# Performance work log

Hardware: AMD Instinct MI355X
Metric: run time of the kernel (lower is better)

The kernel has to match this reference:

```python
import jax, jax.numpy as jnp
import numpy as np

B, R, N, M, K = 4, 4, 4096, 64, 3
F_NUM = 512
KN = K * N


def _block(x, Ws, bs):
    """SO-Net PointResNet: 1x1 convs + ReLU; last layer sees concat(input, hidden)."""
    h = x
    for W, b in zip(Ws[:-1], bs[:-1]):
        h = jax.nn.relu(jnp.einsum('oc,bcn->bon', W, h) + b[None, :, None])
    h = jnp.concatenate([x, h], axis=1)
    return jax.nn.relu(jnp.einsum('oc,bcn->bon', Ws[-1], h) + bs[-1][None, :, None])


def _forward(x, intensity, node, node_knn_I, fpW, fpB, gpW, gpB):
    # --- som.query_topk: k nearest SOM nodes per point ---
    xd = jax.lax.stop_gradient(x)
    dist = jnp.sum((xd[:, :, :, None] - node[:, :, None, :]) ** 2, axis=1)      # B,N,M
    _, topk = jax.lax.top_k(-dist, K)                                           # B,N,K
    min_idx = topk.transpose(0, 2, 1).reshape(B, KN)                            # B,KN (k copies stacked)
    mask = jax.nn.one_hot(min_idx, M, dtype=jnp.float32)                        # B,KN,M
    mask_row_max = jnp.max(mask, axis=1) > 0                                    # B,M  node has >=1 point
    mask_row_sum = jnp.sum(mask, axis=1)                                        # B,M  points per node

    x_stack = jnp.tile(x, (1, 1, K))                                            # B,2,KN
    cluster_mean = jnp.einsum('bcn,bnm->bcm', jax.lax.stop_gradient(x_stack), mask) \
                   / (mask_row_sum[:, None, :] + 1e-5)                          # B,2,M (detached)

    # --- rotation group (2x2 rotations at angles 2*pi*r/R) ---
    theta = 2.0 * jnp.pi * jnp.arange(R, dtype=jnp.float32) / R
    c, s = jnp.cos(theta), jnp.sin(theta)
    rot = jnp.stack([jnp.stack([c, -s], -1), jnp.stack([s, c], -1)], -2)        # R,2,2

    x_rot = jnp.einsum('rij,bjn->brin', rot, x_stack)                           # B,R,2,KN
    node_rot = jnp.einsum('rij,bjm->brim', rot, cluster_mean)                   # B,R,2,M
    centers = jnp.take_along_axis(node_rot, min_idx[:, None, None, :], axis=3)  # B,R,2,KN
    x_dec = jax.lax.stop_gradient(x_rot - centers).reshape(B * R, 2, KN)

    # --- first PointResNet over all B*R rotation copies ---
    feat = _block(x_dec, fpW, fpB)                                              # BR,128,KN

    # --- index_max scatter-max per SOM cluster (value of argmax == segment max) ---
    seg = jnp.tile(min_idx[:, None, :], (1, R, 1)).reshape(B * R, KN)
    segmax = jax.vmap(lambda f, sgi: jax.ops.segment_max(f.T, sgi, num_segments=M).T)(feat, seg)
    rowmax = jnp.tile(mask_row_max[:, None, :], (1, R, 1)).reshape(B * R, M)
    pooled = jnp.where(rowmax[:, None, :], segmax, feat[:, :, 0:1])             # BR,128,M (empty -> gather idx 0)

    # --- final PointResNet over SOM nodes, then max over nodes and rotations ---
    g_in = jnp.concatenate([node_rot.reshape(B * R, 2, M), pooled], axis=1)     # BR,130,M
    out = _block(g_in, gpW, gpB)                                                # BR,F,M
    return out.reshape(B, R, F_NUM, M).max(axis=3).max(axis=1)                  # B,F


def setup_inputs() -> dict:
    key = jax.random.key(0)
    ks = jax.random.split(key, 24)
    d = {}
    d['x'] = jax.random.normal(ks[0], (B, 2, N), jnp.float32)
    d['intensity'] = jax.random.uniform(ks[1], (B, 1, N), jnp.float32)
    d['node'] = jax.random.normal(ks[2], (B, 2, M), jnp.float32)
    d['node_knn_I'] = jax.random.randint(ks[3], (B, M, 1), 0, M)
    dims_fp = [(64, 2), (64, 64), (128, 64), (128, 130)]      # PointResNet(2,[64,64,128,128])
    dims_gp = [(256, 130), (256, 256), (512, 256), (F_NUM, 642)]  # PointResNet(130,[256,256,512,F])
    i = 4
    for name, dims in (('fp', dims_fp), ('gp', dims_gp)):
        for j, (o, ci) in enumerate(dims):
            d[f'{name}_W{j}'] = jax.random.normal(ks[i], (o, ci), jnp.float32) / np.sqrt(ci).astype(np.float32)
            d[f'{name}_b{j}'] = jnp.zeros((o,), jnp.float32)
            i += 1
    return d


def reference(x, intensity, node, node_knn_I,
              fp_W0, fp_b0, fp_W1, fp_b1, fp_W2, fp_b2, fp_W3, fp_b3,
              gp_W0, gp_b0, gp_W1, gp_b1, gp_W2, gp_b2, gp_W3, gp_b3):
    return _forward(x, intensity, node, node_knn_I,
                    [fp_W0, fp_W1, fp_W2, fp_W3], [fp_b0, fp_b1, fp_b2, fp_b3],
                    [gp_W0, gp_W1, gp_W2, gp_W3], [gp_b0, gp_b1, gp_b2, gp_b3])
```

## Files before the change

### kernel.cpp

```cpp
#include <hip/hip_runtime.h>
#include <stdint.h>

#define BB 4
#define RR 4
#define NN 4096
#define MM 64
#define KK 3
#define KNN 12288
#define BRR 16
#define FF 512

#define W_FPW1 0
#define W_FPW2 4096
#define W_FPW3 12288
#define W_GPW0 28928
#define W_GPW1 62208
#define W_GPW2 127744
#define W_GPW3 258816
#define W_FPB1 587520
#define W_FPB2 587584
#define W_FPB3 587712
#define W_GPB0 587840
#define W_GPB1 588096
#define W_GPB2 588352
#define W_GPB3 588864
#define W_FPB0 589376
#define W_FPW0 589440
#define W_TOT  589568

typedef short bf16x8 __attribute__((ext_vector_type(8)));
typedef float f32x4 __attribute__((ext_vector_type(4)));

__device__ __forceinline__ float bf2f(unsigned int u) {
  union { unsigned int i; float f; } v; v.i = u << 16; return v.f;
}
__device__ __forceinline__ unsigned short f2bf(float f) {
  union { float f; unsigned int i; } v; v.f = f;
  unsigned int x = v.i;
  return (unsigned short)((x + 0x7fffu + ((x >> 16) & 1u)) >> 16);
}
__device__ __forceinline__ unsigned int f2bf2(float a, float b) {
#if __has_builtin(__builtin_amdgcn_cvt_pk_bf16_f32)
  typedef __bf16 bf2_t __attribute__((ext_vector_type(2)));
  union { bf2_t v; unsigned int u; } c;
  c.v = __builtin_amdgcn_cvt_pk_bf16_f32(a, b);
  return c.u;
#else
  return (unsigned int)f2bf(a) | ((unsigned int)f2bf(b) << 16);
#endif
}
__device__ __forceinline__ float ldf(const void* p, long i, int isbf) {
  if (isbf) return bf2f(((const unsigned short*)p)[i]);
  return ((const float*)p)[i];
}
__device__ __forceinline__ int detect_bf(const unsigned short* xs) {
  int lane = threadIdx.x & 63;
  unsigned short u = xs[lane * 2];
  int e = (u >> 7) & 0xFF;
  int bad = (e >= 0x90 || (e > 0 && e <= 0x50)) ? 1 : 0;
  unsigned long long m = __ballot(bad);
  return __popcll(m) < 16;
}

struct SrcPtrs { const void* p[16]; };
__global__ __launch_bounds__(256) void k_pre(
    SrcPtrs sp, const void* __restrict__ x, const void* __restrict__ node,
    int* __restrict__ idx, float* __restrict__ csum, int* __restrict__ blkcnt,
    unsigned short* __restrict__ Wb, unsigned long long* __restrict__ pooled64) {
  int isbf = detect_bf((const unsigned short*)x);
  int tid = threadIdx.x;
  if (blockIdx.x >= 64) {
    int zb = blockIdx.x - 64;
    if (zb < 256) pooled64[zb * 256 + tid] = 0ull;
    int t2 = zb * 256 + tid;
    int t = t2 * 2;
    if (t >= W_TOT) return;
    int s, base;
    if (t < 28928) {
      if (t < 4096)        { s=0;  base=0; }
      else if (t < 12288)  { s=1;  base=4096; }
      else                 { s=2;  base=12288; }
    } else if (t < 587520) {
      if (t < 62208)       { s=3;  base=28928; }
      else if (t < 127744) { s=4;  base=62208; }
      else if (t < 258816) { s=5;  base=127744; }
      else                 { s=6;  base=258816; }
    } else if (t < 588864) {
      if (t < 587584)      { s=7;  base=587520; }
      else if (t < 587712) { s=8;  base=587584; }
      else if (t < 587840) { s=9;  base=587712; }
      else if (t < 588096) { s=10; base=587840; }
      else if (t < 588352) { s=11; base=588096; }
      else                 { s=12; base=588352; }
    } else {
      if (t < 589376)      { s=13; base=588864; }
      else if (t < 589440) { s=14; base=589376; }
      else                 { s=15; base=589440; }
    }
    int local = t - base;
    unsigned int pk;
    if (isbf) pk = *(const unsigned int*)((const unsigned short*)sp.p[s] + local);
    else {
      const float* fp = (const float*)sp.p[s] + local;
      pk = f2bf2(fp[0], fp[1]);
    }
    *(unsigned int*)(Wb + t) = pk;
    return;
  }
  __shared__ float nd[2][64];
  __shared__ float cs[192];
  int b = blockIdx.x >> 4;
  int n = ((blockIdx.x & 15) << 8) + tid;
  if (tid < 128) nd[tid >> 6][tid & 63] = ldf(node, b * 128 + tid, isbf);
  if (tid < 192) cs[tid] = 0.f;
  __syncthreads();
  float x0 = ldf(x, b * 8192 + n, isbf);
  float x1 = ldf(x, b * 8192 + 4096 + n, isbf);
  float d0 = 1e30f, d1 = 1e30f, d2 = 1e30f;
  int m0 = 0, m1 = 0, m2 = 0;
#pragma unroll 8
  for (int m = 0; m < 64; ++m) {
    float dx = x0 - nd[0][m];
    float dy = x1 - nd[1][m];
    float d = __fmul_rn(dx, dx) + __fmul_rn(dy, dy);
    if (d < d0)      { d2=d1; m2=m1; d1=d0; m1=m0; d0=d; m0=m; }
    else if (d < d1) { d2=d1; m2=m1; d1=d;  m1=m; }
    else if (d < d2) { d2=d;  m2=m; }
  }
  long base = ((long)b * NN + n) * 3;
  idx[base] = m0; idx[base + 1] = m1; idx[base + 2] = m2;
  atomicAdd(&cs[m0*3+0], x0); atomicAdd(&cs[m0*3+1], x1); atomicAdd(&cs[m0*3+2], 1.f);
  atomicAdd(&cs[m1*3+0], x0); atomicAdd(&cs[m1*3+1], x1); atomicAdd(&cs[m1*3+2], 1.f);
  atomicAdd(&cs[m2*3+0], x0); atomicAdd(&cs[m2*3+1], x1); atomicAdd(&cs[m2*3+2], 1.f);
  __syncthreads();
  if (tid < 192) atomicAdd(&csum[b * 192 + tid], cs[tid]);
  if (tid < 64) blkcnt[blockIdx.x * 64 + tid] = (int)cs[tid*3 + 2];
}

__global__ __launch_bounds__(256) void k_mid(
    const float* __restrict__ csum, const int* __restrict__ blkcnt,
    const int* __restrict__ idx,
    float* __restrict__ noderot, int* __restrict__ rowflag,
    int* __restrict__ sorted) {
  __shared__ float cls[192];
  __shared__ int offs[64];
  __shared__ int lbase[64];
  __shared__ int lc[64];
  int tid = threadIdx.x;
  int blk = blockIdx.x;
  int b = blk >> 4, chunk = blk & 15;
  if (tid < 192) cls[tid] = csum[b * 192 + tid];
  __syncthreads();
  if (tid < 64) {
    int m = tid;
    float s0 = cls[m*3], s1 = cls[m*3+1], c = cls[m*3+2];
    float mx = s0 / (c + 1e-5f), my = s1 / (c + 1e-5f);
    rowflag[b*64 + m] = (c > 0.f) ? 1 : 0;
    for (int r = 0; r < 4; ++r) {
      float th = 1.5707964f * (float)r;
      float cr = cosf(th), sr = sinf(th);
      noderot[((b*4+r)*2+0)*64 + m] = cr*mx - sr*my;
      noderot[((b*4+r)*2+1)*64 + m] = sr*mx + cr*my;
    }
    lc[m] = 0;
  }
  if (tid == 0) {
    int acc = 0;
    for (int mm = 0; mm < 64; ++mm) { offs[mm] = acc; acc += (int)cls[mm*3+2]; }
  }
  __syncthreads();
  if (tid < 64) {
    int base = offs[tid];
    for (int c2 = 0; c2 < chunk; ++c2) base += blkcnt[(b*16 + c2)*64 + tid];
    lbase[tid] = base;
  }
  __syncthreads();
  int n = (chunk << 8) + tid;
#pragma unroll
  for (int kk = 0; kk < 3; ++kk) {
    int m = idx[((long)b*NN + n)*3 + kk];
    int pos = atomicAdd(&lc[m], 1);
    sorted[b*KNN + lbase[m] + pos] = (m << 12) | n;
  }
}

__global__ __launch_bounds__(512, 6) void k_fused(
    const void* __restrict__ x, const int* __restrict__ sorted,
    const int* __restrict__ idx, const float* __restrict__ noderot,
    const unsigned short* __restrict__ Wb,
    unsigned int* __restrict__ pooled, float* __restrict__ feat0) {
  __shared__ unsigned short Cs[128 * 136];
  __shared__ unsigned short Hs[128 * 72];
  const unsigned short* fW1 = Wb + W_FPW1;
  const unsigned short* fW2 = Wb + W_FPW2;
  const unsigned short* fW3 = Wb + W_FPW3;
  const unsigned short* fb1 = Wb + W_FPB1;
  const unsigned short* fb2 = Wb + W_FPB2;
  const unsigned short* fb3 = Wb + W_FPB3;
  const unsigned short* fb0 = Wb + W_FPB0;
  const unsigned short* fW0 = Wb + W_FPW0;
  int isbf = detect_bf((const unsigned short*)x);
  int tid = threadIdx.x, lane = tid & 63, wv = tid >> 6;
  int quad = lane >> 4, lr = lane & 15;
  int br = blockIdx.y, b = br >> 2, r = br & 3;
  if (tid < 128) {
    int e = sorted[b * KNN + blockIdx.x * 128 + tid];
    int m = e >> 12, n = e & 4095;
    int isz = (n == 0 && m == idx[(long)b * NN * 3]) ? 256 : 0;
    Cs[tid * 136 + 130] = (unsigned short)(m | isz);
    float x0 = ldf(x, b*8192 + n, isbf), x1 = ldf(x, b*8192 + 4096 + n, isbf);
    float th = 1.5707964f * (float)r;
    float cr = cosf(th), sr = sinf(th);
    float xd0 = (cr*x0 - sr*x1) - noderot[(br*2 + 0)*64 + m];
    float xd1 = (sr*x0 + cr*x1) - noderot[(br*2 + 1)*64 + m];
    *(unsigned int*)&Cs[tid * 136] = f2bf2(xd0, xd1);
  }
  __syncthreads();
  {
    int col = tid & 127, og = (tid >> 7) << 4;
    unsigned int xu = *(unsigned int*)&Cs[col * 136];
    float fx0 = bf2f(xu & 0xffff), fx1 = bf2f(xu >> 16);
    union { unsigned int u[8]; bf16x8 v[2]; } o8;
#pragma unroll
    for (int j = 0; j < 16; j += 2) {
      int o = og + j;
      unsigned int wu0 = *(const unsigned int*)&fW0[o*2];
      unsigned int wu1 = *(const unsigned int*)&fW0[o*2 + 2];
      float h0 = bf2f(fb0[o])   + bf2f(wu0 & 0xffff)*fx0 + bf2f(wu0 >> 16)*fx1;
      float h1 = bf2f(fb0[o+1]) + bf2f(wu1 & 0xffff)*fx0 + bf2f(wu1 >> 16)*fx1;
      o8.u[j >> 1] = f2bf2(fmaxf(h0, 0.f), fmaxf(h1, 0.f));
    }
    *(bf16x8*)&Hs[col*72 + og]     = o8.v[0];
    *(bf16x8*)&Hs[col*72 + og + 8] = o8.v[1];
  }
  __syncthreads();
  {
    int o0 = (wv & 3) * 16, cb = (wv >> 2) * 64;
    f32x4 acc[4];
    float bb4[4];
#pragma unroll
    for (int rr = 0; rr < 4; ++rr) bb4[rr] = bf2f(fb1[o0 + quad*4 + rr]);
#pragma unroll
    for (int nt = 0; nt < 4; ++nt) acc[nt] = (f32x4){bb4[0], bb4[1], bb4[2], bb4[3]};
#pragma unroll
    for (int ks = 0; ks < 64; ks += 32) {
      bf16x8 a = *(const bf16x8*)(fW1 + (o0 + lr)*64 + ks + quad*8);
#pragma unroll
      for (int nt = 0; nt < 4; ++nt) {
        bf16x8 bf = *(bf16x8*)&Hs[(cb + nt*16 + lr)*72 + ks + quad*8];
        acc[nt] = __builtin_amdgcn_mfma_f32_16x16x32_bf16(a, bf, acc[nt], 0, 0, 0);
      }
    }
    __syncthreads();
#pragma unroll
    for (int nt = 0; nt < 4; ++nt) {
      int col = cb + nt*16 + lr;
      unsigned long long pk =
        (unsigned long long)f2bf2(fmaxf(acc[nt][0],0.f), fmaxf(acc[nt][1],0.f)) |
        ((unsigned long long)f2bf2(fmaxf(acc[nt][2],0.f), fmaxf(acc[nt][3],0.f)) << 32);
      *(unsigned long long*)&Hs[col*72 + o0 + quad*4] = pk;
    }
  }
  __syncthreads();
  {
    int o0 = wv * 16;
    f32x4 acc[8];
    float bb4[4];
#pragma unroll
    for (int rr = 0; rr < 4; ++rr) bb4[rr] = bf2f(fb2[o0 + quad*4 + rr]);
#pragma unroll
    for (int nt = 0; nt < 8; ++nt) acc[nt] = (f32x4){bb4[0], bb4[1], bb4[2], bb4[3]};
#pragma unroll
    for (int ks = 0; ks < 64; ks += 32) {
      bf16x8 a = *(const bf16x8*)(fW2 + (o0 + lr)*64 + ks + quad*8);
#pragma unroll
      for (int nt = 0; nt < 8; ++nt) {
        bf16x8 bf = *(bf16x8*)&Hs[(nt*16 + lr)*72 + ks + quad*8];
        acc[nt] = __builtin_amdgcn_mfma_f32_16x16x32_bf16(a, bf, acc[nt], 0, 0, 0);
      }
    }
#pragma unroll
    for (int nt = 0; nt < 8; ++nt) {
      int col = nt*16 + lr;
      int o = o0 + quad*4;
      *(unsigned int*)&Cs[col*136 + 2 + o] = f2bf2(fmaxf(acc[nt][0],0.f), fmaxf(acc[nt][1],0.f));
      *(unsigned int*)&Cs[col*136 + 4 + o] = f2bf2(fmaxf(acc[nt][2],0.f), fmaxf(acc[nt][3],0.f));
    }
  }
  __syncthreads();
  f32x4 acc3[8];
  {
    int o0 = wv * 16;
    float bb4[4];
#pragma unroll
    for (int rr = 0; rr < 4; ++rr) bb4[rr] = bf2f(fb3[o0 + quad*4 + rr]);
#pragma unroll
    for (int nt = 0; nt < 8; ++nt) acc3[nt] = (f32x4){bb4[0], bb4[1], bb4[2], bb4[3]};
#pragma unroll
    for (int ks = 0; ks < 128; ks += 32) {
      union { bf16x8 v; unsigned int u[4]; } au;
      const unsigned int* ap = (const unsigned int*)(fW3 + (long)(o0 + lr)*130 + ks + quad*8);
      au.u[0] = ap[0]; au.u[1] = ap[1]; au.u[2] = ap[2]; au.u[3] = ap[3];
#pragma unroll
      for (int nt = 0; nt < 8; ++nt) {
        bf16x8 bf = *(bf16x8*)&Cs[(nt*16 + lr)*136 + ks + quad*8];
        acc3[nt] = __builtin_amdgcn_mfma_f32_16x16x32_bf16(au.v, bf, acc3[nt], 0, 0, 0);
      }
    }
    float bu0[8], bu1[8];
#pragma unroll
    for (int nt = 0; nt < 8; ++nt) {
      unsigned int bu = *(unsigned int*)&Cs[(nt*16 + lr)*136 + 128];
      bu0[nt] = bf2f(bu & 0xffff); bu1[nt] = bf2f(bu >> 16);
    }
#pragma unroll
    for (int rr = 0; rr < 4; ++rr) {
      int o = o0 + quad*4 + rr;
      unsigned int wu = *(const unsigned int*)(fW3 + (long)o*130 + 128);
      float w0 = bf2f(wu & 0xffff), w1 = bf2f(wu >> 16);
#pragma unroll
      for (int nt = 0; nt < 8; ++nt)
        acc3[nt][rr] += w0 * bu0[nt] + w1 * bu1[nt];
    }
  }
  __syncthreads();
  {
    int o0 = wv * 16;
#pragma unroll
    for (int nt = 0; nt < 8; ++nt) {
      int col = nt*16 + lr;
      unsigned long long pk =
        (unsigned long long)f2bf2(fmaxf(acc3[nt][0],0.f), fmaxf(acc3[nt][1],0.f)) |
        ((unsigned long long)f2bf2(fmaxf(acc3[nt][2],0.f), fmaxf(acc3[nt][3],0.f)) << 32);
      *(unsigned long long*)&Cs[col*136 + o0 + quad*4] = pk;
    }
  }
  __syncthreads();
  {
    int o = tid & 127, h = tid >> 7;
    int c0 = h * 32;
    float fv[32];
    int mcl[32];
#pragma unroll
    for (int j = 0; j < 32; ++j) {
      fv[j] = bf2f(Cs[(c0 + j)*136 + o]);
      mcl[j] = Cs[(c0 + j)*136 + 130];
    }
    int curm = mcl[0] & 255;
    float v = 0.f;
#pragma unroll
    for (int j = 0; j < 32; ++j) {
      int mm = mcl[j] & 255;
      if (mm != curm) {
        atomicMax(&pooled[(((long)br*64 + curm) << 7) + o], __float_as_uint(v));
        curm = mm; v = 0.f;
      }
      v = fmaxf(v, fv[j]);
      if (mcl[j] & 256) feat0[br*128 + o] = fv[j];
    }
    atomicMax(&pooled[(((long)br*64 + curm) << 7) + o], __float_as_uint(v));
  }
}

__global__ __launch_bounds__(256) void k_fin(
    const unsigned int* __restrict__ pooled, const float* __restrict__ feat0,
    const int* __restrict__ rowflag, const float* __restrict__ noderot,
    unsigned short* __restrict__ AG) {
  int t = blockIdx.x * 256 + threadIdx.x;
  int col = t >> 7, o = t & 127;
  int br = col >> 6, m = col & 63, b = br >> 2;
  float v = __uint_as_float(pooled[((long)col << 7) + o]);
  if (!rowflag[b*64 + m]) v = feat0[br*128 + o];
  AG[(long)col*648 + 2 + o] = f2bf(v);
  if (o < 2) AG[(long)col*648 + o] = f2bf(noderot[(br*2 + o)*64 + m]);
}

template<int KW, int KMAIN, bool REM2, int BSTR, int OSTR, int OOFF, int EPI, bool AAL, int TOTB>
__global__ __launch_bounds__(256) void k_gemm2(
    const unsigned short* __restrict__ W, const unsigned short* __restrict__ Bi,
    const unsigned short* __restrict__ Bb, unsigned short* __restrict__ Out,
    unsigned int* __restrict__ outmax, unsigned int* __restrict__ counter,
    const void* __restrict__ x, void* __restrict__ out) {
  __shared__ int done_s;
  int lane = threadIdx.x & 63, wv = threadIdx.x >> 6;
  int quad = lane >> 4, lr = lane & 15;
  int o0 = blockIdx.y * 64 + wv * 16;
  int p0 = blockIdx.x * 16;
  f32x4 acc;
  {
    int ob = o0 + quad*4;
    acc = (f32x4){bf2f(Bi[ob]), bf2f(Bi[ob+1]), bf2f(Bi[ob+2]), bf2f(Bi[ob+3])};
  }
  const unsigned short* arow = W + (long)(o0 + lr) * KW;
  const unsigned short* brow = Bb + (long)(p0 + lr) * BSTR;
#pragma unroll 4
  for (int ks = 0; ks < KMAIN; ks += 32) {
    bf16x8 a;
    if constexpr (AAL) {
      a = *(const bf16x8*)(arow + ks + quad*8);
    } else {
      union { bf16x8 v; unsigned int u[4]; } au;
      const unsigned int* ap = (const unsigned int*)(arow + ks + quad*8);
      au.u[0] = ap[0]; au.u[1] = ap[1]; au.u[2] = ap[2]; au.u[3] = ap[3];
      a = au.v;
    }
    bf16x8 bf = *(const bf16x8*)(brow + ks + quad*8);
    acc = __builtin_amdgcn_mfma_f32_16x16x32_bf16(a, bf, acc, 0, 0, 0);
  }
  if constexpr (REM2) {
    unsigned int bu = *(const unsigned int*)(brow + KMAIN);
    float b0v = bf2f(bu & 0xffff), b1v = bf2f(bu >> 16);
#pragma unroll
    for (int rr = 0; rr < 4; ++rr) {
      int o = o0 + quad*4 + rr;
      unsigned int wu = *(const unsigned int*)(W + (long)o * KW + KMAIN);
      acc[rr] += bf2f(wu & 0xffff) * b0v + bf2f(wu >> 16) * b1v;
    }
  }
  if constexpr (EPI == 0) {
    unsigned short* op = Out + (long)(p0 + lr) * OSTR + OOFF + o0 + quad*4;
    if constexpr (((OOFF * 2) % 8) == 0) {
      unsigned long long pk =
        (unsigned long long)f2bf2(fmaxf(acc[0],0.f), fmaxf(acc[1],0.f)) |
        ((unsigned long long)f2bf2(fmaxf(acc[2],0.f), fmaxf(acc[3],0.f)) << 32);
      *(unsigned long long*)op = pk;
    } else {
      *(unsigned int*)op       = f2bf2(fmaxf(acc[0],0.f), fmaxf(acc[1],0.f));
      *(unsigned int*)(op + 2) = f2bf2(fmaxf(acc[2],0.f), fmaxf(acc[3],0.f));
    }
  } else {
    int b = blockIdx.x >> 4;
#pragma unroll
    for (int rr = 0; rr < 4; ++rr) {
      float v = fmaxf(acc[rr], 0.f);
      v = fmaxf(v, __shfl_xor(v, 1, 64));
      v = fmaxf(v, __shfl_xor(v, 2, 64));
      v = fmaxf(v, __shfl_xor(v, 4, 64));
      v = fmaxf(v, __shfl_xor(v, 8, 64));
      if (lr == 0) atomicMax(&outmax[b * FF + o0 + quad*4 + rr], __float_as_uint(v));
    }
    __threadfence();
    __syncthreads();
    if (threadIdx.x == 0) done_s = (int)atomicAdd(counter, 1u);
    __syncthreads();
    if (done_s == TOTB - 1) {
      int isbf = detect_bf((const unsigned short*)x);
      for (int t = threadIdx.x; t < 2048; t += 256) {
        float v = __uint_as_float(atomicMax(&outmax[t], 0u));
        if (isbf) ((unsigned short*)out)[t] = f2bf(v);
        else      ((float*)out)[t] = v;
      }
    }
  }
}

extern "C" void kernel_launch(void* const* d_in, const int* in_sizes, int n_in,
                              void* d_out, int out_size, void* d_ws, size_t ws_size,
                              hipStream_t stream) {
  const void* x    = d_in[0];
  const void* node = d_in[2];

  char* ws = (char*)d_ws;
  float*          csum    = (float*)(ws + 0);
  unsigned int*   outmax  = (unsigned int*)(ws + 3072);
  unsigned int*   counter = (unsigned int*)(ws + 11264);
  unsigned int*   pooled  = (unsigned int*)(ws + 11520);
  int*            idx     = (int*)(ws + 535808);
  int*            blkcnt  = (int*)(ws + 732416);
  float*          noderot = (float*)(ws + 748800);
  int*            rowflag = (int*)(ws + 756992);
  int*            sorted  = (int*)(ws + 758016);
  float*          feat0   = (float*)(ws + 954624);
  unsigned short* Wb      = (unsigned short*)(ws + 962816);
  unsigned short* AG      = (unsigned short*)(ws + 2141952);
  unsigned short* Hg1     = (unsigned short*)(ws + 3469056);
  unsigned short* Hg2     = (unsigned short*)(ws + 3993344);

  hipMemsetAsync(ws, 0, 11520, stream);

  SrcPtrs sp;
  sp.p[0]  = d_in[6];
  sp.p[1]  = d_in[8];
  sp.p[2]  = d_in[10];
  sp.p[3]  = d_in[12];
  sp.p[4]  = d_in[14];
  sp.p[5]  = d_in[16];
  sp.p[6]  = d_in[18];
  sp.p[7]  = d_in[7];
  sp.p[8]  = d_in[9];
  sp.p[9]  = d_in[11];
  sp.p[10] = d_in[13];
  sp.p[11] = d_in[15];
  sp.p[12] = d_in[17];
  sp.p[13] = d_in[19];
  sp.p[14] = d_in[5];
  sp.p[15] = d_in[4];

  k_pre<<<64 + (W_TOT/2 + 255) / 256, 256, 0, stream>>>(
      sp, x, node, idx, csum, blkcnt, Wb, (unsigned long long*)pooled);
  k_mid<<<64, 256, 0, stream>>>(csum, blkcnt, idx, noderot, rowflag, sorted);
  k_fused<<<dim3(96, 16), 512, 0, stream>>>(x, sorted, idx, noderot, Wb, pooled, feat0);
  k_fin<<<512, 256, 0, stream>>>(pooled, feat0, rowflag, noderot, AG);

  k_gemm2<130, 128, true, 648, 256, 0, 0, false, 0>
      <<<dim3(64, 4), 256, 0, stream>>>(Wb + W_GPW0, Wb + W_GPB0, AG, Hg1,
                                        nullptr, nullptr, x, nullptr);
  k_gemm2<256, 256, false, 256, 256, 0, 0, true, 0>
      <<<dim3(64, 4), 256, 0, stream>>>(Wb + W_GPW1, Wb + W_GPB1, Hg1, Hg2,
                                        nullptr, nullptr, x, nullptr);
  k_gemm2<256, 256, false, 256, 648, 130, 0, true, 0>
      <<<dim3(64, 8), 256, 0, stream>>>(Wb + W_GPW2, Wb + W_GPB2, Hg2, AG,
                                        nullptr, nullptr, x, nullptr);
  k_gemm2<642, 640, true, 648, 0, 0, 2, false, 512>
      <<<dim3(64, 8), 256, 0, stream>>>(Wb + W_GPW3, Wb + W_GPB3, AG, nullptr,
                                        outmax, counter, x, d_out);
}
```

Measured before the change: 204.2 us.

## Prepack GP weights into k8-blocked zero-padded layout and stage B tiles in LDS

The weight-conversion prologue now writes the point-cloud GEMM weights in a k8-major blocked layout, zero-padded to a multiple of 32 along K. This lets each lane fetch a contiguous, aligned 16-byte A fragment and removes the unaligned scalar loads and the K-remainder scalar tail. The GEMM kernel also stages its 16-column B tile into shared memory once per block before the MFMA loop. The trade-off is extra padded MACs, a barrier per block, and a larger prologue grid and workspace.

Result: no change. 203.8 us (-0.2%).

```diff
diff --git a/kernel.cpp b/kernel.cpp
--- a/kernel.cpp
+++ b/kernel.cpp
@@ -10,23 +10,25 @@
 #define BRR 16
 #define FF 512
 
-#define W_FPW1 0
-#define W_FPW2 4096
-#define W_FPW3 12288
-#define W_GPW0 28928
-#define W_GPW1 62208
-#define W_GPW2 127744
-#define W_GPW3 258816
-#define W_FPB1 587520
-#define W_FPB2 587584
-#define W_FPB3 587712
-#define W_GPB0 587840
-#define W_GPB1 588096
-#define W_GPB2 588352
-#define W_GPB3 588864
-#define W_FPB0 589376
-#define W_FPW0 589440
-#define W_TOT  589568
+#define F_W1 0
+#define F_W2 4096
+#define F_W3 12288
+#define F_B1 28928
+#define F_B2 28992
+#define F_B3 29120
+#define G_B0 29248
+#define G_B1 29504
+#define G_B2 29760
+#define G_B3 30272
+#define F_B0 30784
+#define F_W0 30848
+#define WB2_TOT 30976
+
+#define P_W0 0
+#define P_W1 40960
+#define P_W2 106496
+#define P_W3 237568
+#define WP_TOT 581632
 
 typedef short bf16x8 __attribute__((ext_vector_type(8)));
 typedef float f32x4 __attribute__((ext_vector_type(4)));
@@ -66,45 +68,65 @@
 __global__ __launch_bounds__(256) void k_pre(
     SrcPtrs sp, const void* __restrict__ x, const void* __restrict__ node,
     int* __restrict__ idx, float* __restrict__ csum, int* __restrict__ blkcnt,
-    unsigned short* __restrict__ Wb, unsigned long long* __restrict__ pooled64) {
+    unsigned short* __restrict__ Wb2, unsigned short* __restrict__ Wp,
+    unsigned long long* __restrict__ pooled64) {
   int isbf = detect_bf((const unsigned short*)x);
   int tid = threadIdx.x;
   if (blockIdx.x >= 64) {
     int zb = blockIdx.x - 64;
     if (zb < 256) pooled64[zb * 256 + tid] = 0ull;
-    int t2 = zb * 256 + tid;
-    int t = t2 * 2;
-    if (t >= W_TOT) return;
-    int s, base;
-    if (t < 28928) {
-      if (t < 4096)        { s=0;  base=0; }
-      else if (t < 12288)  { s=1;  base=4096; }
-      else                 { s=2;  base=12288; }
-    } else if (t < 587520) {
-      if (t < 62208)       { s=3;  base=28928; }
-      else if (t < 127744) { s=4;  base=62208; }
-      else if (t < 258816) { s=5;  base=127744; }
-      else                 { s=6;  base=258816; }
-    } else if (t < 588864) {
-      if (t < 587584)      { s=7;  base=587520; }
-      else if (t < 587712) { s=8;  base=587584; }
-      else if (t < 587840) { s=9;  base=587712; }
-      else if (t < 588096) { s=10; base=587840; }
-      else if (t < 588352) { s=11; base=588096; }
-      else                 { s=12; base=588352; }
-    } else {
-      if (t < 589376)      { s=13; base=588864; }
-      else if (t < 589440) { s=14; base=589376; }
-      else                 { s=15; base=589440; }
-    }
+    if (blockIdx.x < 125) {
+      int t = (zb * 256 + tid) * 2;
+      if (t >= WB2_TOT) return;
+      int s, base;
+      if (t < 12288) {
+        if (t < 4096)        { s=0;  base=0; }
+        else                 { s=1;  base=4096; }
+      } else if (t < 28928)  { s=2;  base=12288; }
+      else if (t < 29248) {
+        if (t < 28992)       { s=7;  base=28928; }
+        else if (t < 29120)  { s=8;  base=28992; }
+        else                 { s=9;  base=29120; }
+      } else if (t < 30272) {
+        if (t < 29504)       { s=10; base=29248; }
+        else if (t < 29760)  { s=11; base=29504; }
+        else                 { s=12; base=29760; }
+      } else {
+        if (t < 30784)       { s=13; base=30272; }
+        else if (t < 30848)  { s=14; base=30784; }
+        else                 { s=15; base=30848; }
+      }
+      int local = t - base;
+      unsigned int pk;
+      if (isbf) pk = *(const unsigned int*)((const unsigned short*)sp.p[s] + local);
+      else {
+        const float* fp = (const float*)sp.p[s] + local;
+        pk = f2bf2(fp[0], fp[1]);
+      }
+      *(unsigned int*)(Wb2 + t) = pk;
+      return;
+    }
+    int t = ((blockIdx.x - 125) * 256 + tid) * 2;
+    if (t >= WP_TOT) return;
+    int base, KW, rs; const void* src;
+    if (t < 40960)       { base=0;      KW=130; rs=8; src=sp.p[3]; }
+    else if (t < 106496) { base=40960;  KW=256; rs=8; src=sp.p[4]; }
+    else if (t < 237568) { base=106496; KW=256; rs=9; src=sp.p[5]; }
+    else                 { base=237568; KW=642; rs=9; src=sp.p[6]; }
     int local = t - base;
-    unsigned int pk;
-    if (isbf) pk = *(const unsigned int*)((const unsigned short*)sp.p[s] + local);
-    else {
-      const float* fp = (const float*)sp.p[s] + local;
-      pk = f2bf2(fp[0], fp[1]);
-    }
-    *(unsigned int*)(Wb + t) = pk;
+    int blk = local >> 3, j = local & 7;
+    int k8 = blk >> rs, r = blk & ((1 << rs) - 1);
+    int k = k8 * 8 + j;
+    unsigned int pk = 0u;
+    if (k < KW) {
+      long si = (long)r * KW + k;
+      if (isbf) pk = *(const unsigned int*)((const unsigned short*)src + si);
+      else {
+        const float* fp = (const float*)src + si;
+        pk = f2bf2(fp[0], fp[1]);
+      }
+    }
+    *(unsigned int*)(Wp + t) = pk;
     return;
   }
   __shared__ float nd[2][64];
@@ -187,18 +209,18 @@
 __global__ __launch_bounds__(512, 6) void k_fused(
     const void* __restrict__ x, const int* __restrict__ sorted,
     const int* __restrict__ idx, const float* __restrict__ noderot,
-    const unsigned short* __restrict__ Wb,
+    const unsigned short* __restrict__ Wb2,
     unsigned int* __restrict__ pooled, float* __restrict__ feat0) {
   __shared__ unsigned short Cs[128 * 136];
   __shared__ unsigned short Hs[128 * 72];
-  const unsigned short* fW1 = Wb + W_FPW1;
-  const unsigned short* fW2 = Wb + W_FPW2;
-  const unsigned short* fW3 = Wb + W_FPW3;
-  const unsigned short* fb1 = Wb + W_FPB1;
-  const unsigned short* fb2 = Wb + W_FPB2;
-  const unsigned short* fb3 = Wb + W_FPB3;
-  const unsigned short* fb0 = Wb + W_FPB0;
-  const unsigned short* fW0 = Wb + W_FPW0;
+  const unsigned short* fW1 = Wb2 + F_W1;
+  const unsigned short* fW2 = Wb2 + F_W2;
+  const unsigned short* fW3 = Wb2 + F_W3;
+  const unsigned short* fb1 = Wb2 + F_B1;
+  const unsigned short* fb2 = Wb2 + F_B2;
+  const unsigned short* fb3 = Wb2 + F_B3;
+  const unsigned short* fb0 = Wb2 + F_B0;
+  const unsigned short* fW0 = Wb2 + F_W0;
   int isbf = detect_bf((const unsigned short*)x);
   int tid = threadIdx.x, lane = tid & 63, wv = tid >> 6;
   int quad = lane >> 4, lr = lane & 15;
@@ -375,47 +397,38 @@
   if (o < 2) AG[(long)col*648 + o] = f2bf(noderot[(br*2 + o)*64 + m]);
 }
 
-template<int KW, int KMAIN, bool REM2, int BSTR, int OSTR, int OOFF, int EPI, bool AAL, int TOTB>
-__global__ __launch_bounds__(256) void k_gemm2(
-    const unsigned short* __restrict__ W, const unsigned short* __restrict__ Bi,
+template<int KP, int KREAD, int R, int BSTR, int OSTR, int OOFF, int EPI, int TOTB>
+__global__ __launch_bounds__(256) void k_gemm3(
+    const unsigned short* __restrict__ A, const unsigned short* __restrict__ Bi,
     const unsigned short* __restrict__ Bb, unsigned short* __restrict__ Out,
     unsigned int* __restrict__ outmax, unsigned int* __restrict__ counter,
     const void* __restrict__ x, void* __restrict__ out) {
+  constexpr int KPL = KP + 8;
+  __shared__ unsigned short Bs[16 * KPL];
   __shared__ int done_s;
-  int lane = threadIdx.x & 63, wv = threadIdx.x >> 6;
+  int tid = threadIdx.x;
+  int lane = tid & 63, wv = tid >> 6;
   int quad = lane >> 4, lr = lane & 15;
   int o0 = blockIdx.y * 64 + wv * 16;
   int p0 = blockIdx.x * 16;
+  for (int i = tid; i < 16 * (KP/2); i += 256) {
+    int row = i / (KP/2), kd = i - row * (KP/2);
+    int k = kd * 2;
+    unsigned int v = 0u;
+    if (k < KREAD) v = *(const unsigned int*)(Bb + (long)(p0 + row) * BSTR + k);
+    *(unsigned int*)&Bs[row * KPL + k] = v;
+  }
   f32x4 acc;
   {
     int ob = o0 + quad*4;
     acc = (f32x4){bf2f(Bi[ob]), bf2f(Bi[ob+1]), bf2f(Bi[ob+2]), bf2f(Bi[ob+3])};
   }
-  const unsigned short* arow = W + (long)(o0 + lr) * KW;
-  const unsigned short* brow = Bb + (long)(p0 + lr) * BSTR;
-#pragma unroll 4
-  for (int ks = 0; ks < KMAIN; ks += 32) {
-    bf16x8 a;
-    if constexpr (AAL) {
-      a = *(const bf16x8*)(arow + ks + quad*8);
-    } else {
-      union { bf16x8 v; unsigned int u[4]; } au;
-      const unsigned int* ap = (const unsigned int*)(arow + ks + quad*8);
-      au.u[0] = ap[0]; au.u[1] = ap[1]; au.u[2] = ap[2]; au.u[3] = ap[3];
-      a = au.v;
-    }
-    bf16x8 bf = *(const bf16x8*)(brow + ks + quad*8);
-    acc = __builtin_amdgcn_mfma_f32_16x16x32_bf16(a, bf, acc, 0, 0, 0);
-  }
-  if constexpr (REM2) {
-    unsigned int bu = *(const unsigned int*)(brow + KMAIN);
-    float b0v = bf2f(bu & 0xffff), b1v = bf2f(bu >> 16);
-#pragma unroll
-    for (int rr = 0; rr < 4; ++rr) {
-      int o = o0 + quad*4 + rr;
-      unsigned int wu = *(const unsigned int*)(W + (long)o * KW + KMAIN);
-      acc[rr] += bf2f(wu & 0xffff) * b0v + bf2f(wu >> 16) * b1v;
-    }
+  __syncthreads();
+#pragma unroll
+  for (int ks = 0; ks < KP; ks += 32) {
+    bf16x8 a = *(const bf16x8*)(A + ((ks >> 3) + quad) * (R * 8) + (o0 + lr) * 8);
+    bf16x8 b = *(const bf16x8*)&Bs[lr * KPL + ks + quad * 8];
+    acc = __builtin_amdgcn_mfma_f32_16x16x32_bf16(a, b, acc, 0, 0, 0);
   }
   if constexpr (EPI == 0) {
     unsigned short* op = Out + (long)(p0 + lr) * OSTR + OOFF + o0 + quad*4;
@@ -441,11 +454,11 @@
     }
     __threadfence();
     __syncthreads();
-    if (threadIdx.x == 0) done_s = (int)atomicAdd(counter, 1u);
+    if (tid == 0) done_s = (int)atomicAdd(counter, 1u);
     __syncthreads();
     if (done_s == TOTB - 1) {
       int isbf = detect_bf((const unsigned short*)x);
-      for (int t = threadIdx.x; t < 2048; t += 256) {
+      for (int t = tid; t < 2048; t += 256) {
         float v = __uint_as_float(atomicMax(&outmax[t], 0u));
         if (isbf) ((unsigned short*)out)[t] = f2bf(v);
         else      ((float*)out)[t] = v;
@@ -471,10 +484,11 @@
   int*            rowflag = (int*)(ws + 756992);
   int*            sorted  = (int*)(ws + 758016);
   float*          feat0   = (float*)(ws + 954624);
-  unsigned short* Wb      = (unsigned short*)(ws + 962816);
-  unsigned short* AG      = (unsigned short*)(ws + 2141952);
-  unsigned short* Hg1     = (unsigned short*)(ws + 3469056);
-  unsigned short* Hg2     = (unsigned short*)(ws + 3993344);
+  unsigned short* Wp      = (unsigned short*)(ws + 962816);
+  unsigned short* Wb2     = (unsigned short*)(ws + 2126080);
+  unsigned short* AG      = (unsigned short*)(ws + 2188032);
+  unsigned short* Hg1     = (unsigned short*)(ws + 3515136);
+  unsigned short* Hg2     = (unsigned short*)(ws + 4039424);
 
   hipMemsetAsync(ws, 0, 11520, stream);
 
@@ -496,22 +510,22 @@
   sp.p[14] = d_in[5];
   sp.p[15] = d_in[4];
 
-  k_pre<<<64 + (W_TOT/2 + 255) / 256, 256, 0, stream>>>(
-      sp, x, node, idx, csum, blkcnt, Wb, (unsigned long long*)pooled);
+  k_pre<<<1261, 256, 0, stream>>>(sp, x, node, idx, csum, blkcnt, Wb2, Wp,
+                                  (unsigned long long*)pooled);
   k_mid<<<64, 256, 0, stream>>>(csum, blkcnt, idx, noderot, rowflag, sorted);
-  k_fused<<<dim3(96, 16), 512, 0, stream>>>(x, sorted, idx, noderot, Wb, pooled, feat0);
+  k_fused<<<dim3(96, 16), 512, 0, stream>>>(x, sorted, idx, noderot, Wb2, pooled, feat0);
   k_fin<<<512, 256, 0, stream>>>(pooled, feat0, rowflag, noderot, AG);
 
-  k_gemm2<130, 128, true, 648, 256, 0, 0, false, 0>
-      <<<dim3(64, 4), 256, 0, stream>>>(Wb + W_GPW0, Wb + W_GPB0, AG, Hg1,
+  k_gemm3<160, 130, 256, 648, 256, 0, 0, 0>
+      <<<dim3(64, 4), 256, 0, stream>>>(Wp + P_W0, Wb2 + G_B0, AG, Hg1,
                                         nullptr, nullptr, x, nullptr);
-  k_gemm2<256, 256, false, 256, 256, 0, 0, true, 0>
-      <<<dim3(64, 4), 256, 0, stream>>>(Wb + W_GPW1, Wb + W_GPB1, Hg1, Hg2,
+  k_gemm3<256, 256, 256, 256, 256, 0, 0, 0>
+      <<<dim3(64, 4), 256, 0, stream>>>(Wp + P_W1, Wb2 + G_B1, Hg1, Hg2,
                                         nullptr, nullptr, x, nullptr);
-  k_gemm2<256, 256, false, 256, 648, 130, 0, true, 0>
-      <<<dim3(64, 8), 256, 0, stream>>>(Wb + W_GPW2, Wb + W_GPB2, Hg2, AG,
+  k_gemm3<256, 256, 512, 256, 648, 130, 0, 0>
+      <<<dim3(64, 8), 256, 0, stream>>>(Wp + P_W2, Wb2 + G_B2, Hg2, AG,
                                         nullptr, nullptr, x, nullptr);
-  k_gemm2<642, 640, true, 648, 0, 0, 2, false, 512>
-      <<<dim3(64, 8), 256, 0, stream>>>(Wb + W_GPW3, Wb + W_GPB3, AG, nullptr,
+  k_gemm3<672, 642, 512, 648, 0, 0, 2, 512>
+      <<<dim3(64, 8), 256, 0, stream>>>(Wp + P_W3, Wb2 + G_B3, AG, nullptr,
                                         outmax, counter, x, d_out);
 }
```
